# Optimization experiments

Measured on AMD Instinct MI355X. Metric: run time of the kernel, lower is better.

## Reference

```python
import jax, jax.numpy as jnp
import numpy as np

N_NODES = 20000   # max_childs
N_EDGES = 640000
FEAT = 256        # node_feat_size
HID = 128         # node_hidden_size
NUM_SEM = 57
EDGE_TYPES = 4
EDGE_FEAT = 8


def setup_inputs() -> dict:
    key = jax.random.key(0)
    ks = jax.random.split(key, 10)
    inp = {
        "child_feats": jax.random.normal(ks[0], (1, N_NODES, FEAT + NUM_SEM), jnp.float32),
        "child_exists": jnp.ones((1, N_NODES, 1), jnp.float32),
        "edge_type_onehot": jax.random.uniform(ks[1], (1, N_EDGES, EDGE_TYPES), jnp.float32),
        "edge_feats": jax.random.normal(ks[2], (1, N_EDGES, EDGE_FEAT), jnp.float32),
        "edge_indices": jax.random.randint(ks[3], (1, N_EDGES, 2), 0, N_NODES, jnp.int64 if jax.config.jax_enable_x64 else jnp.int32),
        "W_child": jax.random.normal(ks[4], (FEAT + NUM_SEM, HID), jnp.float32) * 0.05,
        "b_child": jnp.zeros((HID,), jnp.float32),
        "W_edge0": jax.random.normal(ks[5], (2 * HID + EDGE_FEAT + EDGE_TYPES, HID), jnp.float32) * 0.05,
        "b_edge0": jnp.zeros((HID,), jnp.float32),
        "W_edge1": jax.random.normal(ks[6], (2 * HID + EDGE_FEAT + EDGE_TYPES, HID), jnp.float32) * 0.05,
        "b_edge1": jnp.zeros((HID,), jnp.float32),
        "W_parent": jax.random.normal(ks[7], (3 * HID, FEAT), jnp.float32) * 0.05,
        "b_parent": jnp.zeros((FEAT,), jnp.float32),
    }
    return inp


def reference(child_feats, child_exists, edge_type_onehot, edge_feats, edge_indices,
              W_child, b_child, W_edge0, b_edge0, W_edge1, b_edge1, W_parent, b_parent):
    # child_op + existence mask: [1, N, FEAT+NUM_SEM] -> [N, HID]
    h = jax.nn.relu(child_feats @ W_child + b_child) * child_exists
    h = h[0]  # batch_size is hard-coded to 1 in the original module

    # symmetric_type == 'max': pool over children
    iter_parent_feats = [jnp.max(h, axis=0)]

    # edge features: cat(edge_type_onehot, edge_feats) -> [E, ET+EF]
    ef = jnp.concatenate([edge_type_onehot[0], edge_feats[0]], axis=1)
    src = edge_indices[0, :, 0]
    dst = edge_indices[0, :, 1]

    for W, b in ((W_edge0, b_edge0), (W_edge1, b_edge1)):
        # gather -> per-edge MLP: [E, 2*HID + ET + EF] -> [E, HID]
        msg = jax.nn.relu(jnp.concatenate([h[src], h[dst], ef], axis=1) @ W + b)
        # edge_symmetric_type == 'max' with zero-initialized out buffer:
        # result = max(0, segment_max(msg)) per node
        h = jnp.maximum(jax.ops.segment_max(msg, src, num_segments=N_NODES), 0.0)
        iter_parent_feats.append(jnp.max(h, axis=0))

    parent = jnp.concatenate(iter_parent_feats)[None, :]  # [1, 3*HID]
    return jax.nn.relu(parent @ W_parent + b_parent)       # [1, FEAT]
```

## Files before the change

### kernel.cpp

```cpp
#include <hip/hip_runtime.h>

#define N_NODES   20000
#define N_EDGES   640000
#define CF        313
#define KC        320
#define ROWB      640

typedef __attribute__((ext_vector_type(8))) short short8;
typedef __attribute__((ext_vector_type(4))) float f32x4;
typedef __attribute__((ext_vector_type(4))) unsigned short u16x4;
typedef _Float16 h2 __attribute__((ext_vector_type(2)));

static __device__ __forceinline__ unsigned short f2bf(float f) {
    unsigned u = __float_as_uint(f);
    u = u + 0x7FFFu + ((u >> 16) & 1u);
    return (unsigned short)(u >> 16);
}
static __device__ __forceinline__ int pkh(float a, float b) {
    h2 h; h.x = (_Float16)a; h.y = (_Float16)b;
    return __builtin_bit_cast(int, h);
}
static __device__ __forceinline__ h2 bch(int v) { return __builtin_bit_cast(h2, v); }
static __device__ __forceinline__ float dot2f(h2 a, h2 b, float c) {
    return __builtin_amdgcn_fdot2(a, b, c, false);
}

__global__ void setup_kernel(const float* __restrict__ Wc,
                             const float* __restrict__ We0,
                             const float* __restrict__ We1,
                             const int* __restrict__ eidx,
                             const float* __restrict__ cf,
                             unsigned short* __restrict__ WcT,
                             unsigned short* __restrict__ Wab0,
                             unsigned short* __restrict__ Wab1,
                             unsigned* __restrict__ hist,
                             unsigned short* __restrict__ cfp) {
    const int b = blockIdx.x, tid = threadIdx.x;
    if (b < 416) {
        int g = b * 256 + tid;
        if (g < 128 * KC) {
            int n = g / KC, k = g % KC;
            WcT[g] = f2bf(k < CF ? Wc[k * 128 + n] : 0.f);
        } else if (g < 128 * KC + 32768) {
            int h = g - 128 * KC;
            int n = h >> 7, k = h & 127;
            Wab0[h] = f2bf(n < 128 ? We0[k * 128 + n] : We0[(128 + k) * 128 + (n - 128)]);
        } else {
            int h = g - 128 * KC - 32768;
            int n = h >> 7, k = h & 127;
            Wab1[h] = f2bf(n < 128 ? We1[k * 128 + n] : We1[(128 + k) * 128 + (n - 128)]);
        }
    } else if (b < 2916) {
        int e = (b - 416) * 256 + tid;
        if (e < N_EDGES) atomicAdd(hist + eidx[2 * e], 1u);
    } else {
        int g = (b - 2916) * 256 + tid;
        if (g < 800000) {
            int node = g / 40, c = g - node * 40;
            const float* base = cf + (size_t)node * CF + c * 8;
            short8 v = {};
            if (c < 39) {
                #pragma unroll
                for (int kk = 0; kk < 8; ++kk) v[kk] = (short)f2bf(base[kk]);
            } else {
                v[0] = (short)f2bf(base[0]);
            }
            *(short8*)(cfp + (size_t)g * 8) = v;
        }
    }
}

__global__ void scan_kernel(const unsigned* __restrict__ hist,
                            unsigned* __restrict__ cursor,
                            unsigned* __restrict__ cstart,
                            unsigned* __restrict__ parent) {
    __shared__ unsigned part[1024];
    int t = threadIdx.x;
    if (t < 384) parent[t] = 0;
    unsigned loc[20];
    unsigned s = 0;
    int base = t * 20;
    if (t < 1000) {
        #pragma unroll
        for (int i = 0; i < 20; ++i) { loc[i] = hist[base + i]; s += loc[i]; }
    }
    part[t] = s;
    __syncthreads();
    for (int off = 1; off < 1024; off <<= 1) {
        unsigned u = (t >= off) ? part[t - off] : 0u;
        __syncthreads();
        part[t] += u;
        __syncthreads();
    }
    if (t < 1000) {
        unsigned run = part[t] - s;
        #pragma unroll
        for (int i = 0; i < 20; ++i) {
            cursor[base + i] = run;
            cstart[base + i] = run;
            run += loc[i];
        }
    }
}

__global__ void scatter_kernel(const int* __restrict__ eidx,
                               const float* __restrict__ onehot,
                               const float* __restrict__ efeat,
                               unsigned* __restrict__ cursor,
                               int4* __restrict__ es) {
    int e = blockIdx.x * 256 + threadIdx.x;
    if (e >= N_EDGES) return;
    int2 sd = ((const int2*)eidx)[e];
    unsigned pos = atomicAdd(cursor + sd.x, 1u);
    float4 oh = *(const float4*)(onehot + 4 * (size_t)e);
    float4 ea = *(const float4*)(efeat + 8 * (size_t)e);
    float4 eb = *(const float4*)(efeat + 8 * (size_t)e + 4);
    int4 w0, w1;
    w0.x = sd.y;
    w0.y = pkh(oh.x, oh.y); w0.z = pkh(oh.z, oh.w); w0.w = pkh(ea.x, ea.y);
    w1.x = pkh(ea.z, ea.w); w1.y = pkh(eb.x, eb.y); w1.z = pkh(eb.z, eb.w);
    w1.w = 0;
    es[2 * (size_t)pos]     = w0;
    es[2 * (size_t)pos + 1] = w1;
}

__global__ __launch_bounds__(256, 2)
void child_gemm(const unsigned short* __restrict__ cfp,
                const float* __restrict__ exists,
                const unsigned short* __restrict__ WT,
                const float* __restrict__ bias,
                unsigned short* __restrict__ hbf,
                unsigned int* __restrict__ pmax) {
    __shared__ __align__(16) unsigned char Alds[64 * ROWB];

    const int tid  = threadIdx.x;
    const int lane = tid & 63;
    const int wave = tid >> 6;
    const int n0   = wave * 32;
    const int row0 = blockIdx.x * 64;

    short8 bfrag[10][2];
    {
        int col  = n0 + (lane & 15);
        int krow = (lane >> 4) * 8;
        #pragma unroll
        for (int ks = 0; ks < 10; ++ks)
            #pragma unroll
            for (int nt = 0; nt < 2; ++nt)
                bfrag[ks][nt] = *(const short8*)(WT + (col + nt * 16) * KC + ks * 32 + krow);
    }
    float bv[2];
    bv[0] = bias[n0 + (lane & 15)];
    bv[1] = bias[n0 + 16 + (lane & 15)];

    {
        int r = tid >> 2, p = tid & 3;
        int node = row0 + r;
        bool valid = node < N_NODES;
        unsigned rbase = r * ROWB;
        unsigned sw = (r & 7) << 4;
        #pragma unroll
        for (int i = 0; i < 10; ++i) {
            int c = p + i * 4;
            short8 v = {};
            if (valid) v = *(const short8*)(cfp + (size_t)node * KC + c * 8);
            *(short8*)(Alds + ((rbase + c * 16) ^ sw)) = v;
        }
    }
    __syncthreads();

    f32x4 acc[4][2] = {};
    {
        int arow = lane & 15;
        unsigned kb = (lane >> 4) * 16;
        #pragma unroll
        for (int ks = 0; ks < 10; ++ks)
            #pragma unroll
            for (int mt = 0; mt < 4; ++mt) {
                int row = mt * 16 + arow;
                short8 a = *(const short8*)(Alds + (((unsigned)row * ROWB + ks * 64 + kb) ^ ((row & 7) << 4)));
                acc[mt][0] = __builtin_amdgcn_mfma_f32_16x16x32_bf16(a, bfrag[ks][0], acc[mt][0], 0, 0, 0);
                acc[mt][1] = __builtin_amdgcn_mfma_f32_16x16x32_bf16(a, bfrag[ks][1], acc[mt][1], 0, 0, 0);
            }
    }

    {
        int rb = (lane >> 4) * 4;
        #pragma unroll
        for (int nt = 0; nt < 2; ++nt) {
            int col = n0 + nt * 16 + (lane & 15);
            float m = 0.f;
            #pragma unroll
            for (int mt = 0; mt < 4; ++mt)
                #pragma unroll
                for (int j = 0; j < 4; ++j) {
                    int node = row0 + mt * 16 + rb + j;
                    float v = 0.f;
                    if (node < N_NODES) {
                        v = fmaxf(acc[mt][nt][j] + bv[nt], 0.f) * exists[node];
                        hbf[node * 128 + col] = f2bf(v);
                    }
                    m = fmaxf(m, v);
                }
            m = fmaxf(m, __shfl_xor(m, 16));
            m = fmaxf(m, __shfl_xor(m, 32));
            if ((lane >> 4) == 0)
                atomicMax(pmax + col, __float_as_uint(m));
        }
    }
}

__global__ __launch_bounds__(256)
void gemmAB(const unsigned short* __restrict__ hbf,
            const unsigned short* __restrict__ WT,
            const float* __restrict__ bias,
            float* __restrict__ Afl,
            unsigned short* __restrict__ Bbf) {
    const int tid  = threadIdx.x;
    const int lane = tid & 63;
    const int wave = tid >> 6;
    const int n0   = wave * 64;
    const int row0 = blockIdx.x * 64;
    const int krow = (lane >> 4) * 8;

    short8 bfrag[4][4];
    {
        int colb = n0 + (lane & 15);
        #pragma unroll
        for (int ks = 0; ks < 4; ++ks)
            #pragma unroll
            for (int nt = 0; nt < 4; ++nt)
                bfrag[ks][nt] = *(const short8*)(WT + (colb + nt * 16) * 128 + ks * 32 + krow);
    }

    f32x4 acc[4][4] = {};
    #pragma unroll
    for (int ks = 0; ks < 4; ++ks)
        #pragma unroll
        for (int mt = 0; mt < 4; ++mt) {
            int row = row0 + mt * 16 + (lane & 15);
            row = min(row, N_NODES - 1);
            short8 a = *(const short8*)(hbf + (size_t)row * 128 + ks * 32 + krow);
            #pragma unroll
            for (int nt = 0; nt < 4; ++nt)
                acc[mt][nt] = __builtin_amdgcn_mfma_f32_16x16x32_bf16(a, bfrag[ks][nt], acc[mt][nt], 0, 0, 0);
        }

    {
        int rb = (lane >> 4) * 4;
        #pragma unroll
        for (int nt = 0; nt < 4; ++nt) {
            int col = n0 + nt * 16 + (lane & 15);
            float badd = (col < 128) ? bias[col] : 0.f;
            #pragma unroll
            for (int mt = 0; mt < 4; ++mt)
                #pragma unroll
                for (int j = 0; j < 4; ++j) {
                    int row = row0 + mt * 16 + rb + j;
                    if (row < N_NODES) {
                        float v = acc[mt][nt][j] + badd;
                        if (col < 128) Afl[(size_t)row * 128 + col] = v;
                        else           Bbf[(size_t)row * 128 + col - 128] = f2bf(v);
                    }
                }
        }
    }
}

__global__ __launch_bounds__(256, 3)
void edge_pass(const unsigned short* __restrict__ Bbf,
               const float* __restrict__ Afl,
               const int4* __restrict__ es,
               const float* __restrict__ Wef,
               const unsigned* __restrict__ cstart,
               const unsigned* __restrict__ hist,
               unsigned short* __restrict__ hbf,
               unsigned* __restrict__ pslice) {
    __shared__ unsigned cmax[128];
    const int tid = threadIdx.x;
    if (tid < 128) cmax[tid] = 0;
    __syncthreads();

    const int s  = blockIdx.x * 8 + (tid >> 5);
    const int c0 = (tid & 31) * 4;

    float4 a = *(const float4*)(Afl + (size_t)s * 128 + c0);

    h2 wf[6][4];
    #pragma unroll
    for (int kp = 0; kp < 6; ++kp)
        #pragma unroll
        for (int j = 0; j < 4; ++j) {
            h2 w;
            w.x = (_Float16)Wef[(2 * kp) * 128 + c0 + j];
            w.y = (_Float16)Wef[(2 * kp + 1) * 128 + c0 + j];
            wf[kp][j] = w;
        }

    float m0 = -1e30f, m1 = -1e30f, m2 = -1e30f, m3 = -1e30f;
    const unsigned cnt = hist[s];
    if (cnt) {
        const unsigned last = cnt - 1;
        const unsigned cb = cstart[s] * 32u;
        const char* esb = (const char*)es;
        const unsigned short* bbase = Bbf + c0;

        unsigned dstv[12];
        int4 ra[3], rb[3];
        u16x4 bv[6];

        #pragma unroll
        for (int k = 0; k < 12; ++k)
            dstv[k] = *(const unsigned*)(esb + cb + min((unsigned)k, last) * 32u);
        #pragma unroll
        for (int k = 0; k < 3; ++k) {
            const int4* q = (const int4*)(esb + cb + min((unsigned)k, last) * 32u);
            ra[k] = q[0]; rb[k] = q[1];
        }
        #pragma unroll
        for (int k = 0; k < 6; ++k)
            bv[k] = *(const u16x4*)(bbase + (size_t)dstv[k] * 128);

        const unsigned niter = (cnt + 11) / 12;
        for (unsigned it = 0; it < niter; ++it) {
            const unsigned jb = it * 12;
            #pragma unroll
            for (int u = 0; u < 12; ++u) {
                int4 RA = ra[u % 3], RB = rb[u % 3];
                u16x4 B = bv[u % 6];
                h2 e0 = bch(RA.y), e1 = bch(RA.z), e2 = bch(RA.w);
                h2 e3 = bch(RB.x), e4 = bch(RB.y), e5 = bch(RB.z);

                float x0 = __uint_as_float(((unsigned)(unsigned short)B[0]) << 16);
                float x1 = __uint_as_float(((unsigned)(unsigned short)B[1]) << 16);
                float x2 = __uint_as_float(((unsigned)(unsigned short)B[2]) << 16);
                float x3 = __uint_as_float(((unsigned)(unsigned short)B[3]) << 16);
                x0 = dot2f(e0, wf[0][0], x0); x1 = dot2f(e0, wf[0][1], x1);
                x2 = dot2f(e0, wf[0][2], x2); x3 = dot2f(e0, wf[0][3], x3);
                x0 = dot2f(e1, wf[1][0], x0); x1 = dot2f(e1, wf[1][1], x1);
                x2 = dot2f(e1, wf[1][2], x2); x3 = dot2f(e1, wf[1][3], x3);
                x0 = dot2f(e2, wf[2][0], x0); x1 = dot2f(e2, wf[2][1], x1);
                x2 = dot2f(e2, wf[2][2], x2); x3 = dot2f(e2, wf[2][3], x3);
                x0 = dot2f(e3, wf[3][0], x0); x1 = dot2f(e3, wf[3][1], x1);
                x2 = dot2f(e3, wf[3][2], x2); x3 = dot2f(e3, wf[3][3], x3);
                x0 = dot2f(e4, wf[4][0], x0); x1 = dot2f(e4, wf[4][1], x1);
                x2 = dot2f(e4, wf[4][2], x2); x3 = dot2f(e4, wf[4][3], x3);
                x0 = dot2f(e5, wf[5][0], x0); x1 = dot2f(e5, wf[5][1], x1);
                x2 = dot2f(e5, wf[5][2], x2); x3 = dot2f(e5, wf[5][3], x3);
                m0 = fmaxf(m0, x0); m1 = fmaxf(m1, x1);
                m2 = fmaxf(m2, x2); m3 = fmaxf(m3, x3);

                unsigned jd = min(jb + u + 12u, last);
                dstv[u] = *(const unsigned*)(esb + cb + jd * 32u);
                unsigned jr = min(jb + u + 3u, last);
                const int4* q = (const int4*)(esb + cb + jr * 32u);
                ra[u % 3] = q[0]; rb[u % 3] = q[1];
                bv[u % 6] = *(const u16x4*)(bbase + (size_t)dstv[(u + 6) % 12] * 128);
            }
        }
    }

    float h0 = fmaxf(a.x + m0, 0.f), h1 = fmaxf(a.y + m1, 0.f);
    float h2v = fmaxf(a.z + m2, 0.f), h3 = fmaxf(a.w + m3, 0.f);

    unsigned lo = (unsigned)f2bf(h0) | ((unsigned)f2bf(h1) << 16);
    unsigned hi = (unsigned)f2bf(h2v) | ((unsigned)f2bf(h3) << 16);
    *(uint2*)(hbf + (size_t)s * 128 + c0) = make_uint2(lo, hi);

    float g0 = fmaxf(h0, __shfl_xor(h0, 32));
    float g1 = fmaxf(h1, __shfl_xor(h1, 32));
    float g2 = fmaxf(h2v, __shfl_xor(h2v, 32));
    float g3 = fmaxf(h3, __shfl_xor(h3, 32));
    if ((tid & 63) < 32) {
        atomicMax(&cmax[c0],     __float_as_uint(g0));
        atomicMax(&cmax[c0 + 1], __float_as_uint(g1));
        atomicMax(&cmax[c0 + 2], __float_as_uint(g2));
        atomicMax(&cmax[c0 + 3], __float_as_uint(g3));
    }
    __syncthreads();
    if (tid < 128) atomicMax(pslice + tid, cmax[tid]);
}

__global__ void final_gemm(const float* __restrict__ parent,
                           const float* __restrict__ Wp,
                           const float* __restrict__ bp,
                           float* __restrict__ out) {
    __shared__ float p[384];
    __shared__ float red[1024];
    int t = threadIdx.x;
    if (t < 384) p[t] = parent[t];
    __syncthreads();
    int col = t & 255, kc = t >> 8;
    float s = 0.f;
    for (int k = kc * 96; k < kc * 96 + 96; ++k) s += p[k] * Wp[k * 256 + col];
    red[t] = s;
    __syncthreads();
    if (kc == 0)
        out[col] = fmaxf(red[col] + red[col + 256] + red[col + 512] + red[col + 768] + bp[col], 0.f);
}

extern "C" void kernel_launch(void* const* d_in, const int* in_sizes, int n_in,
                              void* d_out, int out_size, void* d_ws, size_t ws_size,
                              hipStream_t stream) {
    const float* child_feats  = (const float*)d_in[0];
    const float* child_exists = (const float*)d_in[1];
    const float* onehot       = (const float*)d_in[2];
    const float* efeat        = (const float*)d_in[3];
    const int*   eidx         = (const int*)d_in[4];
    const float* Wc  = (const float*)d_in[5];
    const float* bc  = (const float*)d_in[6];
    const float* We0 = (const float*)d_in[7];
    const float* be0 = (const float*)d_in[8];
    const float* We1 = (const float*)d_in[9];
    const float* be1 = (const float*)d_in[10];
    const float* Wp  = (const float*)d_in[11];
    const float* bp  = (const float*)d_in[12];

    char* ws = (char*)d_ws;
    unsigned short* hbf    = (unsigned short*)(ws);
    float*          Afl    = (float*)(ws + 5120000);
    unsigned short* Bbf    = (unsigned short*)(ws + 15360000);
    int4*           es     = (int4*)(ws + 20480000);
    unsigned short* cfp    = (unsigned short*)(ws + 40960000);
    unsigned short* WcT    = (unsigned short*)(ws + 53760000);
    unsigned short* Wab0   = (unsigned short*)(ws + 53841920);
    unsigned short* Wab1   = (unsigned short*)(ws + 53907456);
    unsigned*       parent = (unsigned*)(ws + 53972992);
    unsigned*       hist   = (unsigned*)(ws + 53974528);
    unsigned*       cstart = (unsigned*)(ws + 54054528);
    unsigned*       cursor = (unsigned*)(ws + 54134592);

    const float* Wef0 = We0 + 256 * 128;
    const float* Wef1 = We1 + 256 * 128;

    hipMemsetAsync(hist, 0, N_NODES * 4, stream);

    setup_kernel<<<6041, 256, 0, stream>>>(Wc, We0, We1, eidx, child_feats,
                                           WcT, Wab0, Wab1, hist, cfp);
    scan_kernel<<<1, 1024, 0, stream>>>(hist, cursor, cstart, parent);
    child_gemm<<<313, 256, 0, stream>>>(cfp, child_exists, WcT, bc, hbf, parent);
    scatter_kernel<<<2500, 256, 0, stream>>>(eidx, onehot, efeat, cursor, es);

    gemmAB<<<313, 256, 0, stream>>>(hbf, Wab0, be0, Afl, Bbf);
    edge_pass<<<2500, 256, 0, stream>>>(Bbf, Afl, es, Wef0, cstart, hist, hbf, parent + 128);

    gemmAB<<<313, 256, 0, stream>>>(hbf, Wab1, be1, Afl, Bbf);
    edge_pass<<<2500, 256, 0, stream>>>(Bbf, Afl, es, Wef1, cstart, hist, hbf, parent + 256);

    final_gemm<<<1, 1024, 0, stream>>>((const float*)parent, Wp, bp, (float*)d_out);
}
```

Before: 278.3 us.

## Fuse child-feature bf16 conversion into child GEMM and remap edge pass to wave-per-node

Removes the separate pass that converted child features to a padded bf16 buffer and instead converts the fp32 rows directly while loading them into LDS in child_gemm. This saves a full write and read of the intermediate, at the cost of scalar strided fp32 loads in the GEMM prologue. The edge pass now gives each node a full 64-lane wave with 2 columns per lane instead of a half-wave with 4, which doubles the grid and raises launch bounds to 4. It also restructures the gather prefetch into a double-buffered batch of 12 neighbor loads per iteration, to expose more memory parallelism on the irregular gathers.

```diff
diff --git a/kernel.cpp b/kernel.cpp
--- a/kernel.cpp
+++ b/kernel.cpp
@@ -8,7 +8,6 @@
 
 typedef __attribute__((ext_vector_type(8))) short short8;
 typedef __attribute__((ext_vector_type(4))) float f32x4;
-typedef __attribute__((ext_vector_type(4))) unsigned short u16x4;
 typedef _Float16 h2 __attribute__((ext_vector_type(2)));
 
 static __device__ __forceinline__ unsigned short f2bf(float f) {
@@ -29,12 +28,10 @@
                              const float* __restrict__ We0,
                              const float* __restrict__ We1,
                              const int* __restrict__ eidx,
-                             const float* __restrict__ cf,
                              unsigned short* __restrict__ WcT,
                              unsigned short* __restrict__ Wab0,
                              unsigned short* __restrict__ Wab1,
-                             unsigned* __restrict__ hist,
-                             unsigned short* __restrict__ cfp) {
+                             unsigned* __restrict__ hist) {
     const int b = blockIdx.x, tid = threadIdx.x;
     if (b < 416) {
         int g = b * 256 + tid;
@@ -50,23 +47,9 @@
             int n = h >> 7, k = h & 127;
             Wab1[h] = f2bf(n < 128 ? We1[k * 128 + n] : We1[(128 + k) * 128 + (n - 128)]);
         }
-    } else if (b < 2916) {
+    } else {
         int e = (b - 416) * 256 + tid;
         if (e < N_EDGES) atomicAdd(hist + eidx[2 * e], 1u);
-    } else {
-        int g = (b - 2916) * 256 + tid;
-        if (g < 800000) {
-            int node = g / 40, c = g - node * 40;
-            const float* base = cf + (size_t)node * CF + c * 8;
-            short8 v = {};
-            if (c < 39) {
-                #pragma unroll
-                for (int kk = 0; kk < 8; ++kk) v[kk] = (short)f2bf(base[kk]);
-            } else {
-                v[0] = (short)f2bf(base[0]);
-            }
-            *(short8*)(cfp + (size_t)g * 8) = v;
-        }
     }
 }
 
@@ -125,7 +108,7 @@
 }
 
 __global__ __launch_bounds__(256, 2)
-void child_gemm(const unsigned short* __restrict__ cfp,
+void child_gemm(const float* __restrict__ cf,
                 const float* __restrict__ exists,
                 const unsigned short* __restrict__ WT,
                 const float* __restrict__ bias,
@@ -157,13 +140,20 @@
         int r = tid >> 2, p = tid & 3;
         int node = row0 + r;
         bool valid = node < N_NODES;
+        const float* g = cf + (size_t)node * CF;
         unsigned rbase = r * ROWB;
         unsigned sw = (r & 7) << 4;
         #pragma unroll
         for (int i = 0; i < 10; ++i) {
             int c = p + i * 4;
             short8 v = {};
-            if (valid) v = *(const short8*)(cfp + (size_t)node * KC + c * 8);
+            if (valid) {
+                #pragma unroll
+                for (int kk = 0; kk < 8; ++kk) {
+                    int k = c * 8 + kk;
+                    if (k < CF) v[kk] = (short)f2bf(g[k]);
+                }
+            }
             *(short8*)(Alds + ((rbase + c * 16) ^ sw)) = v;
         }
     }
@@ -267,7 +257,7 @@
     }
 }
 
-__global__ __launch_bounds__(256, 3)
+__global__ __launch_bounds__(256, 4)
 void edge_pass(const unsigned short* __restrict__ Bbf,
                const float* __restrict__ Afl,
                const int4* __restrict__ es,
@@ -281,102 +271,95 @@
     if (tid < 128) cmax[tid] = 0;
     __syncthreads();
 
-    const int s  = blockIdx.x * 8 + (tid >> 5);
-    const int c0 = (tid & 31) * 4;
-
-    float4 a = *(const float4*)(Afl + (size_t)s * 128 + c0);
-
-    h2 wf[6][4];
+    const int s    = blockIdx.x * 4 + (tid >> 6);
+    const int lane = tid & 63;
+    const int c0   = lane * 2;
+
+    float2 a = *(const float2*)(Afl + (size_t)s * 128 + c0);
+
+    h2 wf[6][2];
     #pragma unroll
     for (int kp = 0; kp < 6; ++kp)
         #pragma unroll
-        for (int j = 0; j < 4; ++j) {
+        for (int j = 0; j < 2; ++j) {
             h2 w;
             w.x = (_Float16)Wef[(2 * kp) * 128 + c0 + j];
             w.y = (_Float16)Wef[(2 * kp + 1) * 128 + c0 + j];
             wf[kp][j] = w;
         }
 
-    float m0 = -1e30f, m1 = -1e30f, m2 = -1e30f, m3 = -1e30f;
+    float m0 = -1e30f, m1 = -1e30f;
     const unsigned cnt = hist[s];
     if (cnt) {
         const unsigned last = cnt - 1;
-        const unsigned cb = cstart[s] * 32u;
-        const char* esb = (const char*)es;
+        const char* seg = (const char*)es + (size_t)cstart[s] * 32u;
         const unsigned short* bbase = Bbf + c0;
 
-        unsigned dstv[12];
-        int4 ra[3], rb[3];
-        u16x4 bv[6];
-
+        unsigned bcur[12];
+        unsigned dnext[12];
+        int4 ra[4], rb[4];
+
+        #pragma unroll
+        for (int k = 0; k < 12; ++k) {
+            unsigned d = *(const unsigned*)(seg + (size_t)min((unsigned)k, last) * 32u);
+            bcur[k] = *(const unsigned*)(bbase + (size_t)d * 128);
+        }
         #pragma unroll
         for (int k = 0; k < 12; ++k)
-            dstv[k] = *(const unsigned*)(esb + cb + min((unsigned)k, last) * 32u);
-        #pragma unroll
-        for (int k = 0; k < 3; ++k) {
-            const int4* q = (const int4*)(esb + cb + min((unsigned)k, last) * 32u);
+            dnext[k] = *(const unsigned*)(seg + (size_t)min((unsigned)(12 + k), last) * 32u);
+        #pragma unroll
+        for (int k = 0; k < 4; ++k) {
+            const int4* q = (const int4*)(seg + (size_t)min((unsigned)k, last) * 32u);
             ra[k] = q[0]; rb[k] = q[1];
         }
-        #pragma unroll
-        for (int k = 0; k < 6; ++k)
-            bv[k] = *(const u16x4*)(bbase + (size_t)dstv[k] * 128);
 
         const unsigned niter = (cnt + 11) / 12;
         for (unsigned it = 0; it < niter; ++it) {
             const unsigned jb = it * 12;
+
+            unsigned bnext[12], dnn[12];
+            #pragma unroll
+            for (int k = 0; k < 12; ++k)
+                bnext[k] = *(const unsigned*)(bbase + (size_t)dnext[k] * 128);
+            #pragma unroll
+            for (int k = 0; k < 12; ++k)
+                dnn[k] = *(const unsigned*)(seg + (size_t)min(jb + 24u + k, last) * 32u);
+
             #pragma unroll
             for (int u = 0; u < 12; ++u) {
-                int4 RA = ra[u % 3], RB = rb[u % 3];
-                u16x4 B = bv[u % 6];
+                int4 RA = ra[u & 3], RB = rb[u & 3];
+                unsigned B = bcur[u];
                 h2 e0 = bch(RA.y), e1 = bch(RA.z), e2 = bch(RA.w);
                 h2 e3 = bch(RB.x), e4 = bch(RB.y), e5 = bch(RB.z);
 
-                float x0 = __uint_as_float(((unsigned)(unsigned short)B[0]) << 16);
-                float x1 = __uint_as_float(((unsigned)(unsigned short)B[1]) << 16);
-                float x2 = __uint_as_float(((unsigned)(unsigned short)B[2]) << 16);
-                float x3 = __uint_as_float(((unsigned)(unsigned short)B[3]) << 16);
+                float x0 = __uint_as_float(B << 16);
+                float x1 = __uint_as_float(B & 0xffff0000u);
                 x0 = dot2f(e0, wf[0][0], x0); x1 = dot2f(e0, wf[0][1], x1);
-                x2 = dot2f(e0, wf[0][2], x2); x3 = dot2f(e0, wf[0][3], x3);
                 x0 = dot2f(e1, wf[1][0], x0); x1 = dot2f(e1, wf[1][1], x1);
-                x2 = dot2f(e1, wf[1][2], x2); x3 = dot2f(e1, wf[1][3], x3);
                 x0 = dot2f(e2, wf[2][0], x0); x1 = dot2f(e2, wf[2][1], x1);
-                x2 = dot2f(e2, wf[2][2], x2); x3 = dot2f(e2, wf[2][3], x3);
                 x0 = dot2f(e3, wf[3][0], x0); x1 = dot2f(e3, wf[3][1], x1);
-                x2 = dot2f(e3, wf[3][2], x2); x3 = dot2f(e3, wf[3][3], x3);
                 x0 = dot2f(e4, wf[4][0], x0); x1 = dot2f(e4, wf[4][1], x1);
-                x2 = dot2f(e4, wf[4][2], x2); x3 = dot2f(e4, wf[4][3], x3);
                 x0 = dot2f(e5, wf[5][0], x0); x1 = dot2f(e5, wf[5][1], x1);
-                x2 = dot2f(e5, wf[5][2], x2); x3 = dot2f(e5, wf[5][3], x3);
                 m0 = fmaxf(m0, x0); m1 = fmaxf(m1, x1);
-                m2 = fmaxf(m2, x2); m3 = fmaxf(m3, x3);
-
-                unsigned jd = min(jb + u + 12u, last);
-                dstv[u] = *(const unsigned*)(esb + cb + jd * 32u);
-                unsigned jr = min(jb + u + 3u, last);
-                const int4* q = (const int4*)(esb + cb + jr * 32u);
-                ra[u % 3] = q[0]; rb[u % 3] = q[1];
-                bv[u % 6] = *(const u16x4*)(bbase + (size_t)dstv[(u + 6) % 12] * 128);
+
+                unsigned jr = min(jb + u + 4u, last);
+                const int4* q = (const int4*)(seg + (size_t)jr * 32u);
+                ra[u & 3] = q[0]; rb[u & 3] = q[1];
             }
-        }
-    }
-
-    float h0 = fmaxf(a.x + m0, 0.f), h1 = fmaxf(a.y + m1, 0.f);
-    float h2v = fmaxf(a.z + m2, 0.f), h3 = fmaxf(a.w + m3, 0.f);
-
-    unsigned lo = (unsigned)f2bf(h0) | ((unsigned)f2bf(h1) << 16);
-    unsigned hi = (unsigned)f2bf(h2v) | ((unsigned)f2bf(h3) << 16);
-    *(uint2*)(hbf + (size_t)s * 128 + c0) = make_uint2(lo, hi);
-
-    float g0 = fmaxf(h0, __shfl_xor(h0, 32));
-    float g1 = fmaxf(h1, __shfl_xor(h1, 32));
-    float g2 = fmaxf(h2v, __shfl_xor(h2v, 32));
-    float g3 = fmaxf(h3, __shfl_xor(h3, 32));
-    if ((tid & 63) < 32) {
-        atomicMax(&cmax[c0],     __float_as_uint(g0));
-        atomicMax(&cmax[c0 + 1], __float_as_uint(g1));
-        atomicMax(&cmax[c0 + 2], __float_as_uint(g2));
-        atomicMax(&cmax[c0 + 3], __float_as_uint(g3));
-    }
+
+            #pragma unroll
+            for (int k = 0; k < 12; ++k) { bcur[k] = bnext[k]; dnext[k] = dnn[k]; }
+        }
+    }
+
+    float h0 = fmaxf(a.x + m0, 0.f);
+    float h1 = fmaxf(a.y + m1, 0.f);
+
+    *(unsigned*)(hbf + (size_t)s * 128 + c0) =
+        (unsigned)f2bf(h0) | ((unsigned)f2bf(h1) << 16);
+
+    atomicMax(&cmax[c0],     __float_as_uint(h0));
+    atomicMax(&cmax[c0 + 1], __float_as_uint(h1));
     __syncthreads();
     if (tid < 128) atomicMax(pslice + tid, cmax[tid]);
 }
@@ -421,31 +404,29 @@
     float*          Afl    = (float*)(ws + 5120000);
     unsigned short* Bbf    = (unsigned short*)(ws + 15360000);
     int4*           es     = (int4*)(ws + 20480000);
-    unsigned short* cfp    = (unsigned short*)(ws + 40960000);
-    unsigned short* WcT    = (unsigned short*)(ws + 53760000);
-    unsigned short* Wab0   = (unsigned short*)(ws + 53841920);
-    unsigned short* Wab1   = (unsigned short*)(ws + 53907456);
-    unsigned*       parent = (unsigned*)(ws + 53972992);
-    unsigned*       hist   = (unsigned*)(ws + 53974528);
-    unsigned*       cstart = (unsigned*)(ws + 54054528);
-    unsigned*       cursor = (unsigned*)(ws + 54134592);
+    unsigned short* WcT    = (unsigned short*)(ws + 40960000);
+    unsigned short* Wab0   = (unsigned short*)(ws + 41041920);
+    unsigned short* Wab1   = (unsigned short*)(ws + 41107456);
+    unsigned*       parent = (unsigned*)(ws + 41172992);
+    unsigned*       hist   = (unsigned*)(ws + 41174528);
+    unsigned*       cstart = (unsigned*)(ws + 41254528);
+    unsigned*       cursor = (unsigned*)(ws + 41334592);
 
     const float* Wef0 = We0 + 256 * 128;
     const float* Wef1 = We1 + 256 * 128;
 
     hipMemsetAsync(hist, 0, N_NODES * 4, stream);
 
-    setup_kernel<<<6041, 256, 0, stream>>>(Wc, We0, We1, eidx, child_feats,
-                                           WcT, Wab0, Wab1, hist, cfp);
+    setup_kernel<<<2916, 256, 0, stream>>>(Wc, We0, We1, eidx, WcT, Wab0, Wab1, hist);
     scan_kernel<<<1, 1024, 0, stream>>>(hist, cursor, cstart, parent);
-    child_gemm<<<313, 256, 0, stream>>>(cfp, child_exists, WcT, bc, hbf, parent);
+    child_gemm<<<313, 256, 0, stream>>>(child_feats, child_exists, WcT, bc, hbf, parent);
     scatter_kernel<<<2500, 256, 0, stream>>>(eidx, onehot, efeat, cursor, es);
 
     gemmAB<<<313, 256, 0, stream>>>(hbf, Wab0, be0, Afl, Bbf);
-    edge_pass<<<2500, 256, 0, stream>>>(Bbf, Afl, es, Wef0, cstart, hist, hbf, parent + 128);
+    edge_pass<<<5000, 256, 0, stream>>>(Bbf, Afl, es, Wef0, cstart, hist, hbf, parent + 128);
 
     gemmAB<<<313, 256, 0, stream>>>(hbf, Wab1, be1, Afl, Bbf);
-    edge_pass<<<2500, 256, 0, stream>>>(Bbf, Afl, es, Wef1, cstart, hist, hbf, parent + 256);
+    edge_pass<<<5000, 256, 0, stream>>>(Bbf, Afl, es, Wef1, cstart, hist, hbf, parent + 256);
 
     final_gemm<<<1, 1024, 0, stream>>>((const float*)parent, Wp, bp, (float*)d_out);
 }
```

Measured after the change: 383.1 us. +37.6%, slower.

## Fuse child projection with first edge A/B GEMM and convert features in-kernel

Applied to the files above, without the earlier changes.

The separate bf16 conversion pass over child_feats is dropped; the child GEMM now reads fp32 features directly and converts them while staging to LDS. The child GEMM output h stays in LDS and feeds the first layer's A/B projection in the same kernel, removing the hbf round trip and one launch. The final parent GEMM is spread over 16 blocks with a tree reduction instead of a single block. In exchange, the fused kernel uses more LDS and registers (launch bound 2 removed), and unaligned fp32 loads may be less efficient.

```diff
diff --git a/kernel.cpp b/kernel.cpp
--- a/kernel.cpp
+++ b/kernel.cpp
@@ -9,6 +9,7 @@
 typedef __attribute__((ext_vector_type(8))) short short8;
 typedef __attribute__((ext_vector_type(4))) float f32x4;
 typedef __attribute__((ext_vector_type(4))) unsigned short u16x4;
+typedef float f32x4u __attribute__((ext_vector_type(4), aligned(4)));
 typedef _Float16 h2 __attribute__((ext_vector_type(2)));
 
 static __device__ __forceinline__ unsigned short f2bf(float f) {
@@ -29,12 +30,10 @@
                              const float* __restrict__ We0,
                              const float* __restrict__ We1,
                              const int* __restrict__ eidx,
-                             const float* __restrict__ cf,
                              unsigned short* __restrict__ WcT,
                              unsigned short* __restrict__ Wab0,
                              unsigned short* __restrict__ Wab1,
-                             unsigned* __restrict__ hist,
-                             unsigned short* __restrict__ cfp) {
+                             unsigned* __restrict__ hist) {
     const int b = blockIdx.x, tid = threadIdx.x;
     if (b < 416) {
         int g = b * 256 + tid;
@@ -50,23 +49,9 @@
             int n = h >> 7, k = h & 127;
             Wab1[h] = f2bf(n < 128 ? We1[k * 128 + n] : We1[(128 + k) * 128 + (n - 128)]);
         }
-    } else if (b < 2916) {
+    } else {
         int e = (b - 416) * 256 + tid;
         if (e < N_EDGES) atomicAdd(hist + eidx[2 * e], 1u);
-    } else {
-        int g = (b - 2916) * 256 + tid;
-        if (g < 800000) {
-            int node = g / 40, c = g - node * 40;
-            const float* base = cf + (size_t)node * CF + c * 8;
-            short8 v = {};
-            if (c < 39) {
-                #pragma unroll
-                for (int kk = 0; kk < 8; ++kk) v[kk] = (short)f2bf(base[kk]);
-            } else {
-                v[0] = (short)f2bf(base[0]);
-            }
-            *(short8*)(cfp + (size_t)g * 8) = v;
-        }
     }
 }
 
@@ -124,46 +109,62 @@
     es[2 * (size_t)pos + 1] = w1;
 }
 
-__global__ __launch_bounds__(256, 2)
-void child_gemm(const unsigned short* __restrict__ cfp,
-                const float* __restrict__ exists,
-                const unsigned short* __restrict__ WT,
-                const float* __restrict__ bias,
-                unsigned short* __restrict__ hbf,
-                unsigned int* __restrict__ pmax) {
+__global__ __launch_bounds__(256)
+void child_ab(const float* __restrict__ cf,
+              const float* __restrict__ exists,
+              const unsigned short* __restrict__ WcT,
+              const float* __restrict__ bc,
+              const unsigned short* __restrict__ Wab,
+              const float* __restrict__ be,
+              float* __restrict__ Afl,
+              unsigned short* __restrict__ Bbf,
+              unsigned int* __restrict__ pmax) {
     __shared__ __align__(16) unsigned char Alds[64 * ROWB];
+    __shared__ __align__(16) unsigned char Hlds[64 * 256];
 
     const int tid  = threadIdx.x;
     const int lane = tid & 63;
     const int wave = tid >> 6;
-    const int n0   = wave * 32;
     const int row0 = blockIdx.x * 64;
 
+    const int n0c = wave * 32;
     short8 bfrag[10][2];
     {
-        int col  = n0 + (lane & 15);
+        int col  = n0c + (lane & 15);
         int krow = (lane >> 4) * 8;
         #pragma unroll
         for (int ks = 0; ks < 10; ++ks)
             #pragma unroll
             for (int nt = 0; nt < 2; ++nt)
-                bfrag[ks][nt] = *(const short8*)(WT + (col + nt * 16) * KC + ks * 32 + krow);
-    }
-    float bv[2];
-    bv[0] = bias[n0 + (lane & 15)];
-    bv[1] = bias[n0 + 16 + (lane & 15)];
+                bfrag[ks][nt] = *(const short8*)(WcT + (col + nt * 16) * KC + ks * 32 + krow);
+    }
+    float bvc[2];
+    bvc[0] = bc[n0c + (lane & 15)];
+    bvc[1] = bc[n0c + 16 + (lane & 15)];
 
     {
         int r = tid >> 2, p = tid & 3;
         int node = row0 + r;
         bool valid = node < N_NODES;
+        const float* g = cf + (size_t)node * CF;
         unsigned rbase = r * ROWB;
         unsigned sw = (r & 7) << 4;
         #pragma unroll
         for (int i = 0; i < 10; ++i) {
             int c = p + i * 4;
             short8 v = {};
-            if (valid) v = *(const short8*)(cfp + (size_t)node * KC + c * 8);
+            if (valid) {
+                if (c < 39) {
+                    f32x4u a0 = *(const f32x4u*)(g + c * 8);
+                    f32x4u a1 = *(const f32x4u*)(g + c * 8 + 4);
+                    v[0] = (short)f2bf(a0.x); v[1] = (short)f2bf(a0.y);
+                    v[2] = (short)f2bf(a0.z); v[3] = (short)f2bf(a0.w);
+                    v[4] = (short)f2bf(a1.x); v[5] = (short)f2bf(a1.y);
+                    v[6] = (short)f2bf(a1.z); v[7] = (short)f2bf(a1.w);
+                } else {
+                    v[0] = (short)f2bf(g[312]);
+                }
+            }
             *(short8*)(Alds + ((rbase + c * 16) ^ sw)) = v;
         }
     }
@@ -188,24 +189,69 @@
         int rb = (lane >> 4) * 4;
         #pragma unroll
         for (int nt = 0; nt < 2; ++nt) {
-            int col = n0 + nt * 16 + (lane & 15);
+            int col = n0c + nt * 16 + (lane & 15);
             float m = 0.f;
             #pragma unroll
             for (int mt = 0; mt < 4; ++mt)
                 #pragma unroll
                 for (int j = 0; j < 4; ++j) {
-                    int node = row0 + mt * 16 + rb + j;
+                    int r = mt * 16 + rb + j;
+                    int node = row0 + r;
                     float v = 0.f;
-                    if (node < N_NODES) {
-                        v = fmaxf(acc[mt][nt][j] + bv[nt], 0.f) * exists[node];
-                        hbf[node * 128 + col] = f2bf(v);
-                    }
+                    if (node < N_NODES)
+                        v = fmaxf(acc[mt][nt][j] + bvc[nt], 0.f) * exists[node];
+                    *(unsigned short*)(Hlds + (((unsigned)r * 256 + col * 2) ^ ((r & 7) << 4))) = f2bf(v);
                     m = fmaxf(m, v);
                 }
             m = fmaxf(m, __shfl_xor(m, 16));
             m = fmaxf(m, __shfl_xor(m, 32));
             if ((lane >> 4) == 0)
                 atomicMax(pmax + col, __float_as_uint(m));
+        }
+    }
+    __syncthreads();
+
+    const int n0 = wave * 64;
+    const int krow = (lane >> 4) * 8;
+    short8 bfrag2[4][4];
+    {
+        int colb = n0 + (lane & 15);
+        #pragma unroll
+        for (int ks = 0; ks < 4; ++ks)
+            #pragma unroll
+            for (int nt = 0; nt < 4; ++nt)
+                bfrag2[ks][nt] = *(const short8*)(Wab + (colb + nt * 16) * 128 + ks * 32 + krow);
+    }
+
+    f32x4 acc2[4][4] = {};
+    #pragma unroll
+    for (int ks = 0; ks < 4; ++ks)
+        #pragma unroll
+        for (int mt = 0; mt < 4; ++mt) {
+            int r = mt * 16 + (lane & 15);
+            short8 a = *(const short8*)(Hlds + (((unsigned)r * 256 + ks * 64 + krow * 2) ^ ((r & 7) << 4)));
+            #pragma unroll
+            for (int nt = 0; nt < 4; ++nt)
+                acc2[mt][nt] = __builtin_amdgcn_mfma_f32_16x16x32_bf16(a, bfrag2[ks][nt], acc2[mt][nt], 0, 0, 0);
+        }
+
+    {
+        int rb = (lane >> 4) * 4;
+        #pragma unroll
+        for (int nt = 0; nt < 4; ++nt) {
+            int col = n0 + nt * 16 + (lane & 15);
+            float badd = (col < 128) ? be[col] : 0.f;
+            #pragma unroll
+            for (int mt = 0; mt < 4; ++mt)
+                #pragma unroll
+                for (int j = 0; j < 4; ++j) {
+                    int row = row0 + mt * 16 + rb + j;
+                    if (row < N_NODES) {
+                        float v = acc2[mt][nt][j] + badd;
+                        if (col < 128) Afl[(size_t)row * 128 + col] = v;
+                        else           Bbf[(size_t)row * 128 + col - 128] = f2bf(v);
+                    }
+                }
         }
     }
 }
@@ -386,17 +432,22 @@
                            const float* __restrict__ bp,
                            float* __restrict__ out) {
     __shared__ float p[384];
-    __shared__ float red[1024];
+    __shared__ float red[256];
     int t = threadIdx.x;
-    if (t < 384) p[t] = parent[t];
-    __syncthreads();
-    int col = t & 255, kc = t >> 8;
+    for (int i = t; i < 384; i += 256) p[i] = parent[i];
+    __syncthreads();
+    int col = blockIdx.x * 16 + (t & 15);
+    int kc  = t >> 4;
     float s = 0.f;
-    for (int k = kc * 96; k < kc * 96 + 96; ++k) s += p[k] * Wp[k * 256 + col];
+    for (int k = kc * 24; k < kc * 24 + 24; ++k) s += p[k] * Wp[k * 256 + col];
     red[t] = s;
     __syncthreads();
-    if (kc == 0)
-        out[col] = fmaxf(red[col] + red[col + 256] + red[col + 512] + red[col + 768] + bp[col], 0.f);
+    #pragma unroll
+    for (int off = 8; off >= 1; off >>= 1) {
+        if (kc < off) red[t] += red[t + off * 16];
+        __syncthreads();
+    }
+    if (t < 16) out[col] = fmaxf(red[t] + bp[col], 0.f);
 }
 
 extern "C" void kernel_launch(void* const* d_in, const int* in_sizes, int n_in,
@@ -421,31 +472,30 @@
     float*          Afl    = (float*)(ws + 5120000);
     unsigned short* Bbf    = (unsigned short*)(ws + 15360000);
     int4*           es     = (int4*)(ws + 20480000);
-    unsigned short* cfp    = (unsigned short*)(ws + 40960000);
-    unsigned short* WcT    = (unsigned short*)(ws + 53760000);
-    unsigned short* Wab0   = (unsigned short*)(ws + 53841920);
-    unsigned short* Wab1   = (unsigned short*)(ws + 53907456);
-    unsigned*       parent = (unsigned*)(ws + 53972992);
-    unsigned*       hist   = (unsigned*)(ws + 53974528);
-    unsigned*       cstart = (unsigned*)(ws + 54054528);
-    unsigned*       cursor = (unsigned*)(ws + 54134592);
+    unsigned short* WcT    = (unsigned short*)(ws + 40960000);
+    unsigned short* Wab0   = (unsigned short*)(ws + 41041920);
+    unsigned short* Wab1   = (unsigned short*)(ws + 41107456);
+    unsigned*       parent = (unsigned*)(ws + 41172992);
+    unsigned*       hist   = (unsigned*)(ws + 41174528);
+    unsigned*       cstart = (unsigned*)(ws + 41254528);
+    unsigned*       cursor = (unsigned*)(ws + 41334592);
 
     const float* Wef0 = We0 + 256 * 128;
     const float* Wef1 = We1 + 256 * 128;
 
     hipMemsetAsync(hist, 0, N_NODES * 4, stream);
 
-    setup_kernel<<<6041, 256, 0, stream>>>(Wc, We0, We1, eidx, child_feats,
-                                           WcT, Wab0, Wab1, hist, cfp);
+    setup_kernel<<<2916, 256, 0, stream>>>(Wc, We0, We1, eidx, WcT, Wab0, Wab1, hist);
     scan_kernel<<<1, 1024, 0, stream>>>(hist, cursor, cstart, parent);
-    child_gemm<<<313, 256, 0, stream>>>(cfp, child_exists, WcT, bc, hbf, parent);
     scatter_kernel<<<2500, 256, 0, stream>>>(eidx, onehot, efeat, cursor, es);
 
-    gemmAB<<<313, 256, 0, stream>>>(hbf, Wab0, be0, Afl, Bbf);
+    child_ab<<<313, 256, 0, stream>>>(child_feats, child_exists, WcT, bc,
+                                      Wab0, be0, Afl, Bbf, parent);
+
     edge_pass<<<2500, 256, 0, stream>>>(Bbf, Afl, es, Wef0, cstart, hist, hbf, parent + 128);
 
     gemmAB<<<313, 256, 0, stream>>>(hbf, Wab1, be1, Afl, Bbf);
     edge_pass<<<2500, 256, 0, stream>>>(Bbf, Afl, es, Wef1, cstart, hist, hbf, parent + 256);
 
-    final_gemm<<<1, 1024, 0, stream>>>((const float*)parent, Wp, bp, (float*)d_out);
-}
+    final_gemm<<<16, 256, 0, stream>>>((const float*)parent, Wp, bp, (float*)d_out);
+}
```

New measurement: 268.3 us. 3.6% less time.
